# Performance work log

Measured on AMD Instinct MI355X. Metric: run time of the kernel, lower is better.

## Reference

```python
import jax, jax.numpy as jnp
import numpy as np

B, S, D, H, L = 8, 4096, 512, 512, 2


def log_g(x):
    # log of g(x) where g(x) = x + 0.5 for x >= 0 else sigmoid(x)
    return jnp.where(x >= 0, jnp.log(jax.nn.relu(x) + 0.5), -jax.nn.softplus(-x))


def g(x):
    return jnp.where(x >= 0, x + 0.5, jax.nn.sigmoid(x))


def mingru_layer(x, h0, wz, bz, wh, bh):
    """Log-space parallel-scan minGRU layer.
    x: (B,S,Din), h0: (B,1,H) positive (already g-activated).
    wz,wh: (H,Din); bz,bh: (H,). Returns full hidden sequence (B,S,H)."""
    k = jnp.einsum('bsd,hd->bsh', x, wz) + bz          # gate pre-activation
    log_z = -jax.nn.softplus(-k)                        # log sigmoid(k)
    log_coeffs = -jax.nn.softplus(k)                    # log(1 - sigmoid(k))
    log_h_tilde = log_g(jnp.einsum('bsd,hd->bsh', x, wh) + bh)
    log_values = log_z + log_h_tilde                    # log(z * h_tilde)
    log_h0 = jnp.log(h0)                                # (B,1,H)
    # Heinsen associative scan in log space
    a_star = jnp.cumsum(
        jnp.concatenate([jnp.zeros_like(log_h0), log_coeffs], axis=1), axis=1)  # (B,S+1,H)
    log_vals = jnp.concatenate([log_h0, log_values], axis=1)                     # (B,S+1,H)
    log_h = a_star + jax.lax.cumlogsumexp(log_vals - a_star, axis=1)
    return jnp.exp(log_h)[:, 1:]                        # (B,S,H)


def setup_inputs() -> dict:
    key = jax.random.key(0)
    ks = jax.random.split(key, 1 + 4 * L)
    x = jax.random.normal(ks[0], (B, S, D), dtype=jnp.float32)
    inp = {'x': x}
    dims_in = [D] + [H] * (L - 1)
    i = 1
    for l in range(L):
        din = dims_in[l]
        stdv = 1.0 / np.sqrt(din)
        inp[f'wz{l}'] = jax.random.uniform(ks[i], (H, din), minval=-stdv, maxval=stdv); i += 1
        inp[f'bz{l}'] = jax.random.uniform(ks[i], (H,), minval=-stdv, maxval=stdv); i += 1
        inp[f'wh{l}'] = jax.random.uniform(ks[i], (H, din), minval=-stdv, maxval=stdv); i += 1
        inp[f'bh{l}'] = jax.random.uniform(ks[i], (H,), minval=-stdv, maxval=stdv); i += 1
    return inp


def reference(x, wz0, bz0, wh0, bh0, wz1, bz1, wh1, bh1):
    # h is None -> h0 = g(zeros) = 0.5 for every layer
    h0 = jnp.full((B, 1, H), 0.5, dtype=x.dtype)
    params = [(wz0, bz0, wh0, bh0), (wz1, bz1, wh1, bh1)]
    inp = x
    finals = []
    for (wz, bz, wh, bh) in params:
        out = mingru_layer(inp, h0, wz, bz, wh, bh)
        finals.append(out[:, -1:])
        inp = out  # Identity layer transform, no residual, dropout=0
    return out, jnp.stack(finals)  # (B,S,H), (L,B,1,H)
```

## Files before the change

kernel.cpp:

```cpp
#include <hip/hip_runtime.h>
#include <math.h>

#define BB 8
#define SS 4096
#define DD 512
#define HH 512
#define MM (BB*SS)

constexpr int TCH = 64;
constexpr int NC  = SS / TCH;
constexpr int BH  = BB * HH;

constexpr int BM = 128;
constexpr int BN = 64;
constexpr int BK = 64;

typedef short  short8  __attribute__((ext_vector_type(8)));
typedef float  float4v __attribute__((ext_vector_type(4)));

__device__ inline unsigned short f2bf(float f) {
    union { float f; unsigned u; } v; v.f = f;
    unsigned r = v.u + 0x7FFF + ((v.u >> 16) & 1);
    return (unsigned short)(r >> 16);
}
__device__ inline float bf_lo(unsigned u) {
    union { unsigned u; float f; } x; x.u = u << 16; return x.f;
}
__device__ inline float bf_hi(unsigned u) {
    union { unsigned u; float f; } x; x.u = u & 0xffff0000u; return x.f;
}
__device__ inline float fast_rcp(float x) {
    return __builtin_amdgcn_rcpf(x);
}

__device__ inline void async_copy16(const void* g, void* l) {
    __builtin_amdgcn_global_load_lds(
        (const __attribute__((address_space(1))) void*)g,
        (__attribute__((address_space(3))) void*)l, 16, 0, 0);
}

__global__ __launch_bounds__(256)
void conv_all(const float* __restrict__ x,
              const float* __restrict__ w0, const float* __restrict__ w1,
              const float* __restrict__ w2, const float* __restrict__ w3,
              short* __restrict__ Xbf, short* __restrict__ Wbf)
{
    constexpr int XBLK = MM * DD / 8 / 256;
    constexpr int WBLK = HH * DD / 8 / 256;
    const int bid = blockIdx.x;
    const float* src; short* dst; size_t base;
    if (bid < XBLK) {
        src = x; dst = Xbf;
        base = ((size_t)bid * 256 + threadIdx.x) * 8;
    } else {
        const int idx  = bid - XBLK;
        const int wsel = idx / WBLK;
        src = (wsel == 0) ? w0 : (wsel == 1) ? w1 : (wsel == 2) ? w2 : w3;
        dst = Wbf + (size_t)wsel * HH * DD;
        base = ((size_t)(idx % WBLK) * 256 + threadIdx.x) * 8;
    }
    float4 a = *(const float4*)(src + base);
    float4 b = *(const float4*)(src + base + 4);
    short8 r;
    r[0] = f2bf(a.x); r[1] = f2bf(a.y); r[2] = f2bf(a.z); r[3] = f2bf(a.w);
    r[4] = f2bf(b.x); r[5] = f2bf(b.y); r[6] = f2bf(b.z); r[7] = f2bf(b.w);
    *(short8*)(dst + base) = r;
}

__global__ __launch_bounds__(256)
void gemm_gate_mfma(const short* __restrict__ Xg, const short* __restrict__ Wz,
                    const float* __restrict__ bz, const short* __restrict__ Wh,
                    const float* __restrict__ bh, unsigned* __restrict__ AV,
                    float2* __restrict__ cAV)
{
    __shared__ char smem[32768];
    short*    lds    = (short*)smem;
    unsigned* lds_av = (unsigned*)smem;
    constexpr int ZOFF = BM * BK;
    constexpr int HOFF = BM * BK + BN * BK;

    const int t    = threadIdx.x;
    const int wave = t >> 6;
    const int lane = t & 63;
    const int col16 = lane & 15;
    const int quad  = lane >> 4;
    const int wm = wave >> 1;
    const int wn = wave & 1;
    const int m0 = blockIdx.x * BM;
    const int n0 = blockIdx.y * BN;

    float4v accz[4][2], acch[4][2];
    #pragma unroll
    for (int i = 0; i < 4; ++i)
        #pragma unroll
        for (int j = 0; j < 2; ++j) {
            accz[i][j] = (float4v){0.f, 0.f, 0.f, 0.f};
            acch[i][j] = (float4v){0.f, 0.f, 0.f, 0.f};
        }

    const int lr = lane >> 3;
    const int lc = (lane & 7) * 8;

    for (int k0 = 0; k0 < DD; k0 += BK) {
        #pragma unroll
        for (int i = 0; i < 4; ++i) {
            const int r0 = wave * 32 + i * 8;
            async_copy16(Xg + (size_t)(m0 + r0 + lr) * DD + k0 + lc,
                         &lds[r0 * BK]);
        }
        #pragma unroll
        for (int i = 0; i < 2; ++i) {
            const int r0 = wave * 16 + i * 8;
            async_copy16(Wz + (size_t)(n0 + r0 + lr) * DD + k0 + lc,
                         &lds[ZOFF + r0 * BK]);
            async_copy16(Wh + (size_t)(n0 + r0 + lr) * DD + k0 + lc,
                         &lds[HOFF + r0 * BK]);
        }
        __syncthreads();

        #pragma unroll
        for (int kk = 0; kk < 2; ++kk) {
            short8 af[4], bzf[2], bhf[2];
            #pragma unroll
            for (int mi = 0; mi < 4; ++mi)
                af[mi] = *(const short8*)&lds[(wm*64 + mi*16 + col16) * BK + kk*32 + quad*8];
            #pragma unroll
            for (int nj = 0; nj < 2; ++nj) {
                bzf[nj] = *(const short8*)&lds[ZOFF + (wn*32 + nj*16 + col16) * BK + kk*32 + quad*8];
                bhf[nj] = *(const short8*)&lds[HOFF + (wn*32 + nj*16 + col16) * BK + kk*32 + quad*8];
            }
            #pragma unroll
            for (int mi = 0; mi < 4; ++mi)
                #pragma unroll
                for (int nj = 0; nj < 2; ++nj) {
                    accz[mi][nj] = __builtin_amdgcn_mfma_f32_16x16x32_bf16(af[mi], bzf[nj], accz[mi][nj], 0, 0, 0);
                    acch[mi][nj] = __builtin_amdgcn_mfma_f32_16x16x32_bf16(af[mi], bhf[nj], acch[mi][nj], 0, 0, 0);
                }
        }
        __syncthreads();
    }

    #pragma unroll
    for (int nj = 0; nj < 2; ++nj) {
        const int ln = wn*32 + nj*16 + col16;
        const int n  = n0 + ln;
        const float bzn = bz[n], bhn = bh[n];
        #pragma unroll
        for (int mi = 0; mi < 4; ++mi) {
            const int lmb = wm*64 + mi*16 + quad*4;
            #pragma unroll
            for (int reg = 0; reg < 4; ++reg) {
                const float kz = accz[mi][nj][reg] + bzn;
                const float kh = acch[mi][nj][reg] + bhn;
                const float a  = fast_rcp(1.0f + __expf(kz));
                const float sn = fast_rcp(1.0f + __expf(-kh));
                const float ht = (kh >= 0.0f) ? (kh + 0.5f) : sn;
                const float v  = (1.0f - a) * ht;
                lds_av[(lmb + reg) * 64 + ln] = ((unsigned)f2bf(v) << 16) | f2bf(a);
            }
        }
    }
    __syncthreads();

    {
        const int row0 = t >> 4;
        const int col  = (t & 15) * 4;
        #pragma unroll
        for (int i = 0; i < 8; ++i) {
            const int row = row0 + i * 16;
            const uint4 u = *(const uint4*)&lds_av[row * 64 + col];
            *(uint4*)&AV[(size_t)(m0 + row) * HH + n0 + col] = u;
        }
    }

    {
        const int task = t >> 1;
        const int hf   = t & 1;
        const int c    = task >> 6;
        const int ln   = task & 63;
        float prod = 1.0f, hl = 0.0f;
        #pragma unroll 8
        for (int s = 0; s < TCH / 2; ++s) {
            const unsigned u = lds_av[(c * TCH + hf * 32 + s) * 64 + ln];
            const float a = bf_lo(u), v = bf_hi(u);
            hl   = fmaf(a, hl, v);
            prod *= a;
        }
        const float pA = __shfl_xor(prod, 1);
        const float pV = __shfl_xor(hl, 1);
        if (hf == 0) {
            const int b  = m0 >> 12;
            const int cg = ((m0 & 4095) >> 6) + c;
            cAV[(size_t)cg * BH + b * HH + (n0 + ln)] =
                make_float2(prod * pA, fmaf(pA, hl, pV));
        }
    }
}

__global__ __launch_bounds__(256)
void scan_apply_f32(const unsigned* __restrict__ AV,
                    const float2* __restrict__ cAV,
                    float* __restrict__ out, float* __restrict__ finals)
{
    const int h = blockIdx.x * 256 + threadIdx.x;
    const int b = blockIdx.y;
    const int c = blockIdx.z;
    const int ch = b * HH + h;
    float hcur = 0.5f;
    for (int cp = 0; cp < c; ++cp) {
        const float2 s = cAV[(size_t)cp * BH + ch];
        hcur = fmaf(s.x, hcur, s.y);
    }
    size_t base = ((size_t)(b * SS + c * TCH)) * HH + h;
    #pragma unroll 8
    for (int tt = 0; tt < TCH; ++tt) {
        const unsigned u = AV[base];
        hcur = fmaf(bf_lo(u), hcur, bf_hi(u));
        out[base] = hcur;
        base += HH;
    }
    if (c == NC - 1) finals[ch] = hcur;
}

__global__ __launch_bounds__(256)
void scan_apply_bf16(const unsigned* __restrict__ AV,
                     const float2* __restrict__ cAV,
                     short* __restrict__ out, float* __restrict__ finals)
{
    const int h = blockIdx.x * 256 + threadIdx.x;
    const int b = blockIdx.y;
    const int c = blockIdx.z;
    const int ch = b * HH + h;
    float hcur = 0.5f;
    for (int cp = 0; cp < c; ++cp) {
        const float2 s = cAV[(size_t)cp * BH + ch];
        hcur = fmaf(s.x, hcur, s.y);
    }
    size_t base = ((size_t)(b * SS + c * TCH)) * HH + h;
    #pragma unroll 8
    for (int tt = 0; tt < TCH; ++tt) {
        const unsigned u = AV[base];
        hcur = fmaf(bf_lo(u), hcur, bf_hi(u));
        out[base] = (short)f2bf(hcur);
        base += HH;
    }
    if (c == NC - 1) finals[ch] = hcur;
}

extern "C" void kernel_launch(void* const* d_in, const int* in_sizes, int n_in,
                              void* d_out, int out_size, void* d_ws, size_t ws_size,
                              hipStream_t stream)
{
    const float* x   = (const float*)d_in[0];
    const float* wz0 = (const float*)d_in[1];
    const float* bz0 = (const float*)d_in[2];
    const float* wh0 = (const float*)d_in[3];
    const float* bh0 = (const float*)d_in[4];
    const float* wz1 = (const float*)d_in[5];
    const float* bz1 = (const float*)d_in[6];
    const float* wh1 = (const float*)d_in[7];
    const float* bh1 = (const float*)d_in[8];

    float* out    = (float*)d_out;
    float* finals = out + (size_t)MM * HH;

    unsigned* AV  = (unsigned*)d_ws;
    short* Xbf    = (short*)(AV + (size_t)MM * HH);
    short* Wbf    = Xbf + (size_t)MM * DD;
    float2* cAV   = (float2*)(Wbf + (size_t)4 * HH * DD);

    short* Wz0 = Wbf;
    short* Wh0 = Wbf + (size_t)1 * HH * DD;
    short* Wz1 = Wbf + (size_t)2 * HH * DD;
    short* Wh1 = Wbf + (size_t)3 * HH * DD;

    const dim3 gg(MM / BM, HH / BN);
    const dim3 gs(HH / 256, BB, NC);

    conv_all<<<MM * DD / 8 / 256 + 4 * (HH * DD / 8 / 256), 256, 0, stream>>>(
        x, wz0, wh0, wz1, wh1, Xbf, Wbf);

    gemm_gate_mfma <<<gg, 256, 0, stream>>>(Xbf, Wz0, bz0, Wh0, bh0, AV, cAV);
    scan_apply_bf16<<<gs, 256, 0, stream>>>(AV, cAV, Xbf, finals);

    gemm_gate_mfma <<<gg, 256, 0, stream>>>(Xbf, Wz1, bz1, Wh1, bh1, AV, cAV);
    scan_apply_f32 <<<gs, 256, 0, stream>>>(AV, cAV, out, finals + BH);
}
```

Measured before the change: 322.7 us.

## Drop LDS staging in gate GEMM, load fragments directly and scan chunks in registers

Rewrites the fused gate GEMM so each wave loads MFMA operand fragments straight from global memory instead of staging tiles through LDS with async copies and barriers. The N tile doubles to 128, so each wave holds a 64x64 output tile for both the gate and candidate accumulators. The per-chunk scan summary is now computed in registers with cross-lane shuffles instead of through an LDS round trip. This removes LDS traffic and barriers but loses cross-wave operand sharing, increases global/L2 load traffic and register pressure (128 accumulator registers), and the AV stores become narrow scattered 4-byte writes instead of coalesced 16-byte ones.

```diff
diff --git a/kernel.cpp b/kernel.cpp
--- a/kernel.cpp
+++ b/kernel.cpp
@@ -12,8 +12,7 @@
 constexpr int BH  = BB * HH;
 
 constexpr int BM = 128;
-constexpr int BN = 64;
-constexpr int BK = 64;
+constexpr int BN = 128;
 
 typedef short  short8  __attribute__((ext_vector_type(8)));
 typedef float  float4v __attribute__((ext_vector_type(4)));
@@ -31,12 +30,6 @@
 }
 __device__ inline float fast_rcp(float x) {
     return __builtin_amdgcn_rcpf(x);
-}
-
-__device__ inline void async_copy16(const void* g, void* l) {
-    __builtin_amdgcn_global_load_lds(
-        (const __attribute__((address_space(1))) void*)g,
-        (__attribute__((address_space(3))) void*)l, 16, 0, 0);
 }
 
 __global__ __launch_bounds__(256)
@@ -67,18 +60,12 @@
     *(short8*)(dst + base) = r;
 }
 
-__global__ __launch_bounds__(256)
+__global__ __launch_bounds__(256, 2)
 void gemm_gate_mfma(const short* __restrict__ Xg, const short* __restrict__ Wz,
                     const float* __restrict__ bz, const short* __restrict__ Wh,
                     const float* __restrict__ bh, unsigned* __restrict__ AV,
                     float2* __restrict__ cAV)
 {
-    __shared__ char smem[32768];
-    short*    lds    = (short*)smem;
-    unsigned* lds_av = (unsigned*)smem;
-    constexpr int ZOFF = BM * BK;
-    constexpr int HOFF = BM * BK + BN * BK;
-
     const int t    = threadIdx.x;
     const int wave = t >> 6;
     const int lane = t & 63;
@@ -89,65 +76,56 @@
     const int m0 = blockIdx.x * BM;
     const int n0 = blockIdx.y * BN;
 
-    float4v accz[4][2], acch[4][2];
+    const short* ap[4]; const short* zp[4]; const short* hp[4];
+    #pragma unroll
+    for (int mi = 0; mi < 4; ++mi)
+        ap[mi] = Xg + (size_t)(m0 + wm*64 + mi*16 + col16) * DD + quad*8;
+    #pragma unroll
+    for (int nj = 0; nj < 4; ++nj) {
+        zp[nj] = Wz + (size_t)(n0 + wn*64 + nj*16 + col16) * DD + quad*8;
+        hp[nj] = Wh + (size_t)(n0 + wn*64 + nj*16 + col16) * DD + quad*8;
+    }
+
+    float4v accz[4][4], acch[4][4];
     #pragma unroll
     for (int i = 0; i < 4; ++i)
         #pragma unroll
-        for (int j = 0; j < 2; ++j) {
+        for (int j = 0; j < 4; ++j) {
             accz[i][j] = (float4v){0.f, 0.f, 0.f, 0.f};
             acch[i][j] = (float4v){0.f, 0.f, 0.f, 0.f};
         }
 
-    const int lr = lane >> 3;
-    const int lc = (lane & 7) * 8;
-
-    for (int k0 = 0; k0 < DD; k0 += BK) {
-        #pragma unroll
-        for (int i = 0; i < 4; ++i) {
-            const int r0 = wave * 32 + i * 8;
-            async_copy16(Xg + (size_t)(m0 + r0 + lr) * DD + k0 + lc,
-                         &lds[r0 * BK]);
-        }
-        #pragma unroll
-        for (int i = 0; i < 2; ++i) {
-            const int r0 = wave * 16 + i * 8;
-            async_copy16(Wz + (size_t)(n0 + r0 + lr) * DD + k0 + lc,
-                         &lds[ZOFF + r0 * BK]);
-            async_copy16(Wh + (size_t)(n0 + r0 + lr) * DD + k0 + lc,
-                         &lds[HOFF + r0 * BK]);
-        }
-        __syncthreads();
-
-        #pragma unroll
-        for (int kk = 0; kk < 2; ++kk) {
-            short8 af[4], bzf[2], bhf[2];
+    #pragma unroll
+    for (int k = 0; k < DD; k += 32) {
+        short8 af[4], bzf[4], bhf[4];
+        #pragma unroll
+        for (int mi = 0; mi < 4; ++mi) af[mi] = *(const short8*)(ap[mi] + k);
+        #pragma unroll
+        for (int nj = 0; nj < 4; ++nj) {
+            bzf[nj] = *(const short8*)(zp[nj] + k);
+            bhf[nj] = *(const short8*)(hp[nj] + k);
+        }
+        #pragma unroll
+        for (int mi = 0; mi < 4; ++mi)
             #pragma unroll
-            for (int mi = 0; mi < 4; ++mi)
-                af[mi] = *(const short8*)&lds[(wm*64 + mi*16 + col16) * BK + kk*32 + quad*8];
-            #pragma unroll
-            for (int nj = 0; nj < 2; ++nj) {
-                bzf[nj] = *(const short8*)&lds[ZOFF + (wn*32 + nj*16 + col16) * BK + kk*32 + quad*8];
-                bhf[nj] = *(const short8*)&lds[HOFF + (wn*32 + nj*16 + col16) * BK + kk*32 + quad*8];
-            }
-            #pragma unroll
-            for (int mi = 0; mi < 4; ++mi)
-                #pragma unroll
-                for (int nj = 0; nj < 2; ++nj) {
-                    accz[mi][nj] = __builtin_amdgcn_mfma_f32_16x16x32_bf16(af[mi], bzf[nj], accz[mi][nj], 0, 0, 0);
-                    acch[mi][nj] = __builtin_amdgcn_mfma_f32_16x16x32_bf16(af[mi], bhf[nj], acch[mi][nj], 0, 0, 0);
-                }
-        }
-        __syncthreads();
-    }
-
-    #pragma unroll
-    for (int nj = 0; nj < 2; ++nj) {
-        const int ln = wn*32 + nj*16 + col16;
-        const int n  = n0 + ln;
+            for (int nj = 0; nj < 4; ++nj) {
+                accz[mi][nj] = __builtin_amdgcn_mfma_f32_16x16x32_bf16(af[mi], bzf[nj], accz[mi][nj], 0, 0, 0);
+                acch[mi][nj] = __builtin_amdgcn_mfma_f32_16x16x32_bf16(af[mi], bhf[nj], acch[mi][nj], 0, 0, 0);
+            }
+    }
+
+    const int b  = m0 >> 12;
+    const int cg = ((m0 & 4095) >> 6) + wm;
+
+    #pragma unroll
+    for (int nj = 0; nj < 4; ++nj) {
+        const int n = n0 + wn*64 + nj*16 + col16;
         const float bzn = bz[n], bhn = bh[n];
+        float TA[4], TV[4];
         #pragma unroll
         for (int mi = 0; mi < 4; ++mi) {
-            const int lmb = wm*64 + mi*16 + quad*4;
+            const int rowb = m0 + wm*64 + mi*16 + quad*4;
+            float cA_ = 1.0f, cV_ = 0.0f;
             #pragma unroll
             for (int reg = 0; reg < 4; ++reg) {
                 const float kz = accz[mi][nj][reg] + bzn;
@@ -156,44 +134,37 @@
                 const float sn = fast_rcp(1.0f + __expf(-kh));
                 const float ht = (kh >= 0.0f) ? (kh + 0.5f) : sn;
                 const float v  = (1.0f - a) * ht;
-                lds_av[(lmb + reg) * 64 + ln] = ((unsigned)f2bf(v) << 16) | f2bf(a);
-            }
-        }
-    }
-    __syncthreads();
-
-    {
-        const int row0 = t >> 4;
-        const int col  = (t & 15) * 4;
-        #pragma unroll
-        for (int i = 0; i < 8; ++i) {
-            const int row = row0 + i * 16;
-            const uint4 u = *(const uint4*)&lds_av[row * 64 + col];
-            *(uint4*)&AV[(size_t)(m0 + row) * HH + n0 + col] = u;
-        }
-    }
-
-    {
-        const int task = t >> 1;
-        const int hf   = t & 1;
-        const int c    = task >> 6;
-        const int ln   = task & 63;
-        float prod = 1.0f, hl = 0.0f;
-        #pragma unroll 8
-        for (int s = 0; s < TCH / 2; ++s) {
-            const unsigned u = lds_av[(c * TCH + hf * 32 + s) * 64 + ln];
-            const float a = bf_lo(u), v = bf_hi(u);
-            hl   = fmaf(a, hl, v);
-            prod *= a;
-        }
-        const float pA = __shfl_xor(prod, 1);
-        const float pV = __shfl_xor(hl, 1);
-        if (hf == 0) {
-            const int b  = m0 >> 12;
-            const int cg = ((m0 & 4095) >> 6) + c;
-            cAV[(size_t)cg * BH + b * HH + (n0 + ln)] =
-                make_float2(prod * pA, fmaf(pA, hl, pV));
-        }
+                const unsigned pav = ((unsigned)f2bf(v) << 16) | f2bf(a);
+                AV[(size_t)(rowb + reg) * HH + n] = pav;
+                const float ar = bf_lo(pav), vr = bf_hi(pav);
+                cV_ = fmaf(ar, cV_, vr);
+                cA_ *= ar;
+            }
+            TA[mi] = cA_; TV[mi] = cV_;
+        }
+        #pragma unroll
+        for (int mi = 0; mi < 4; ++mi) {
+            {
+                const float As = TA[mi], Vs = TV[mi];
+                const float Ap = __shfl_xor(As, 16), Vp = __shfl_xor(Vs, 16);
+                TA[mi] = As * Ap;
+                TV[mi] = (quad & 1) ? fmaf(As, Vp, Vs) : fmaf(Ap, Vs, Vp);
+            }
+            {
+                const float As = TA[mi], Vs = TV[mi];
+                const float Ap = __shfl_xor(As, 32), Vp = __shfl_xor(Vs, 32);
+                TA[mi] = As * Ap;
+                TV[mi] = (quad & 2) ? fmaf(As, Vp, Vs) : fmaf(Ap, Vs, Vp);
+            }
+        }
+        float CA = TA[0], CV = TV[0];
+        #pragma unroll
+        for (int mi = 1; mi < 4; ++mi) {
+            CV = fmaf(TA[mi], CV, TV[mi]);
+            CA *= TA[mi];
+        }
+        if (quad == 0)
+            cAV[(size_t)cg * BH + b * HH + n] = make_float2(CA, CV);
     }
 }
 
```

New measurement: 392.7 us. 1.22x slower.
